# Kernel tuning notes

Hardware: AMD Instinct MI355X
Metric: run time of the kernel (lower is better)

## Reference

```python
import jax, jax.numpy as jnp
import numpy as np

# FlowNetC correlation hyperparameters (from init_kwargs)
PAD = 20
KS = 1
MD = 20
S1 = 1
S2 = 2
MUL = 1


def setup_inputs() -> dict:
    key = jax.random.key(0)
    k1, k2 = jax.random.split(key)
    B, C, H, W = 8, 256, 96, 128
    input1 = jax.random.normal(k1, (B, C, H, W), dtype=jnp.float32)
    input2 = jax.random.normal(k2, (B, C, H, W), dtype=jnp.float32)
    return {"input1": input1, "input2": input2}


def _correlation(in1, in2):
    b, c, h, w = in1.shape
    p1 = jnp.pad(in1, ((0, 0), (0, 0), (PAD, PAD), (PAD, PAD)))
    p2 = jnp.pad(in2, ((0, 0), (0, 0), (PAD, PAD), (PAD, PAD)))
    hp, wp = h + 2 * PAD, w + 2 * PAD
    out_h = (hp - 2 * MD - KS) // S1 + 1
    out_w = (wp - 2 * MD - KS) // S1 + 1
    d = 2 * MD // S2 + 1  # number of displacement steps per axis (21)

    # fixed center region of input1: [b, c, out_h, out_w]
    region1 = p1[:, :, MD:MD + out_h * S1:S1, MD:MD + out_w * S1:S1]

    offs = (jnp.arange(d) - d // 2) * S2  # displacement offsets
    dys, dxs = jnp.meshgrid(offs, offs, indexing='ij')
    dys = dys.reshape(-1)
    dxs = dxs.reshape(-1)

    def step(carry, dydx):
        dy, dx = dydx
        y0 = MD + dy
        x0 = MD + dx
        valid = (y0 >= 0) & (x0 >= 0) & (y0 + out_h * S1 <= hp) & (x0 + out_w * S1 <= wp)
        reg2 = jax.lax.dynamic_slice(
            p2, (0, 0, y0, x0), (b, c, out_h * S1, out_w * S1)
        )[:, :, ::S1, ::S1]
        corr = (region1 * reg2).sum(axis=1) * MUL  # [b, out_h, out_w]
        corr = jnp.where(valid, corr, jnp.zeros_like(corr))
        return carry, corr

    _, chans = jax.lax.scan(step, None, (dys, dxs))  # [d*d, b, out_h, out_w]
    return jnp.transpose(chans, (1, 0, 2, 3))  # [b, d*d, out_h, out_w]


def reference(input1, input2):
    return _correlation(input1, input2)
```

## Files before the change

kernel.cpp:

```cpp
#include <hip/hip_runtime.h>
#include <stdint.h>

#define B_N   8
#define C_N   256
#define H_N   96
#define W_N   128
#define NCK   8
#define ND    21
#define NK    (ND * ND)

typedef __attribute__((ext_vector_type(8))) short short8;
typedef __attribute__((ext_vector_type(4))) float f32x4;

__device__ char zchunk[12288];

__device__ __forceinline__ uint32_t f2bf(float f) {
  uint32_t u = __builtin_bit_cast(uint32_t, f);
  return (u + 0x7fffu + ((u >> 16) & 1u)) >> 16;
}
__device__ __forceinline__ uint32_t packbf(float lo, float hi) {
  return f2bf(lo) | (f2bf(hi) << 16);
}

__global__ __launch_bounds__(256) void prep(const float* __restrict__ in1,
                                            const float* __restrict__ in2,
                                            unsigned short* __restrict__ Apre,
                                            unsigned short* __restrict__ Bpre) {
  __shared__ float tile[32][W_N + 1];
  int blk = blockIdx.x;
  bool isA = blk < 6144;
  int rblk = isA ? blk : blk - 6144;
  int ck = rblk & 7, bi = rblk >> 3;
  int b = bi / H_N, row = bi % H_N;
  const float* src = (isA ? in1 : in2) + ((size_t)(b * C_N + ck * 32) * H_N + row) * W_N;
  int tid = threadIdx.x;
  for (int idx = tid; idx < 32 * W_N; idx += 256) {
    int c = idx >> 7, j = idx & 127;
    tile[c][j] = src[(size_t)c * (H_N * W_N) + j];
  }
  __syncthreads();
  if (isA) {
    uint32_t* dst = (uint32_t*)Apre + (size_t)rblk * 2048;
    for (int q = tid; q < 2048; q += 256) {
      int e2 = q & 3, ln = (q >> 2) & 63, tp = q >> 8;
      int t = tp >> 1, p = tp & 1;
      int m = ln & 15, kg = ln >> 4;
      int c0 = kg * 8 + 2 * e2;
      int j = 32 * t + 2 * m + p;
      dst[q] = packbf(tile[c0][j], tile[c0 + 1][j]);
    }
  } else {
    uint32_t* dst = (uint32_t*)Bpre + (size_t)rblk * 3072;
    for (int q = tid; q < 3072; q += 256) {
      int e2 = q & 3, ln = (q >> 2) & 63, sp = q >> 8;
      int s = sp >> 1, p = sp & 1;
      int m = ln & 15, kg = ln >> 4;
      int c0 = kg * 8 + 2 * e2;
      int x = 32 * s + 2 * m - 20 + p;
      dst[q] = ((unsigned)x < 128u) ? packbf(tile[c0][x], tile[c0 + 1][x]) : 0u;
    }
  }
}

#define DECL_FRAGS(F) short8 F##_a0, F##_a1, F##_bb0, F##_bb1, F##_bb2, F##_bb3, \
                             F##_bb4, F##_bb5, F##_bb6, F##_bb7, F##_bb8, F##_bb9, F##_bb10, F##_bb11

#define LOADF(F, CK) do {                                                        \
  F##_a0 = *(const short8*)(Ap + (size_t)(CK) * 8192);                           \
  F##_a1 = *(const short8*)(Ap + (size_t)(CK) * 8192 + 2048);                    \
  F##_bb0  = *(const short8*)(Bp0 + (size_t)(CK) * bstr0 + 0 * 2048);            \
  F##_bb1  = *(const short8*)(Bp1 + (size_t)(CK) * bstr1 + 0 * 2048);            \
  F##_bb2  = *(const short8*)(Bp2 + (size_t)(CK) * bstr2 + 0 * 2048);            \
  F##_bb3  = *(const short8*)(Bp0 + (size_t)(CK) * bstr0 + 1 * 2048);            \
  F##_bb4  = *(const short8*)(Bp1 + (size_t)(CK) * bstr1 + 1 * 2048);            \
  F##_bb5  = *(const short8*)(Bp2 + (size_t)(CK) * bstr2 + 1 * 2048);            \
  F##_bb6  = *(const short8*)(Bp0 + (size_t)(CK) * bstr0 + 2 * 2048);            \
  F##_bb7  = *(const short8*)(Bp1 + (size_t)(CK) * bstr1 + 2 * 2048);            \
  F##_bb8  = *(const short8*)(Bp2 + (size_t)(CK) * bstr2 + 2 * 2048);            \
  F##_bb9  = *(const short8*)(Bp0 + (size_t)(CK) * bstr0 + 3 * 2048);            \
  F##_bb10 = *(const short8*)(Bp1 + (size_t)(CK) * bstr1 + 3 * 2048);            \
  F##_bb11 = *(const short8*)(Bp2 + (size_t)(CK) * bstr2 + 3 * 2048);            \
} while (0)

#define MF(a, b, c) __builtin_amdgcn_mfma_f32_16x16x32_bf16(a, b, c, 0, 0, 0)
#define COMPUTE(F) do {                                                          \
  acc[0][0][0] = MF(F##_a0, F##_bb0,  acc[0][0][0]);                             \
  acc[0][1][0] = MF(F##_a0, F##_bb1,  acc[0][1][0]);                             \
  acc[0][2][0] = MF(F##_a0, F##_bb2,  acc[0][2][0]);                             \
  acc[0][0][1] = MF(F##_a0, F##_bb3,  acc[0][0][1]);                             \
  acc[1][0][0] = MF(F##_a1, F##_bb3,  acc[1][0][0]);                             \
  acc[0][1][1] = MF(F##_a0, F##_bb4,  acc[0][1][1]);                             \
  acc[1][1][0] = MF(F##_a1, F##_bb4,  acc[1][1][0]);                             \
  acc[0][2][1] = MF(F##_a0, F##_bb5,  acc[0][2][1]);                             \
  acc[1][2][0] = MF(F##_a1, F##_bb5,  acc[1][2][0]);                             \
  acc[0][0][2] = MF(F##_a0, F##_bb6,  acc[0][0][2]);                             \
  acc[1][0][1] = MF(F##_a1, F##_bb6,  acc[1][0][1]);                             \
  acc[0][1][2] = MF(F##_a0, F##_bb7,  acc[0][1][2]);                             \
  acc[1][1][1] = MF(F##_a1, F##_bb7,  acc[1][1][1]);                             \
  acc[0][2][2] = MF(F##_a0, F##_bb8,  acc[0][2][2]);                             \
  acc[1][2][1] = MF(F##_a1, F##_bb8,  acc[1][2][1]);                             \
  acc[1][0][2] = MF(F##_a1, F##_bb9,  acc[1][0][2]);                             \
  acc[1][1][2] = MF(F##_a1, F##_bb10, acc[1][1][2]);                             \
  acc[1][2][2] = MF(F##_a1, F##_bb11, acc[1][2][2]);                             \
} while (0)

__global__ __launch_bounds__(256, 2) void corr_main(const unsigned short* __restrict__ Apre,
                                                    const unsigned short* __restrict__ Bpre,
                                                    float* __restrict__ out) {
  __shared__ float outl[ND][W_N + 1];

  int h = blockIdx.x;
  int l = (h & 7) * 672 + (h >> 3);
  int c = l / 7, q = l - 7 * c;
  int b = c / 96, i0 = c - 96 * b;
  int gidx = 6 - q;
  int i = i0 + 6 * q; if (i >= H_N) i -= H_N;
  int bi = b * H_N + i;
  int dyb = gidx * 3;

  int tid = threadIdx.x;
  int lane = tid & 63, w = tid >> 6;
  int p = w & 1, th = w >> 1;
  int m = lane & 15, kg = lane >> 4;

  f32x4 acc[2][3][3];
#pragma unroll
  for (int a0i = 0; a0i < 2; ++a0i)
#pragma unroll
    for (int a1i = 0; a1i < 3; ++a1i)
#pragma unroll
      for (int a2i = 0; a2i < 3; ++a2i) acc[a0i][a1i][a2i] = {0.f, 0.f, 0.f, 0.f};

  const char* Ap = (const char*)Apre + (size_t)bi * 65536
                   + ((4 * th + p) << 10) + lane * 16;
  const char* Bp0; const char* Bp1; const char* Bp2;
  int bstr0, bstr1, bstr2;
  {
    int y0 = i + 2 * dyb - 20;
#pragma unroll
    for (int g = 0; g < 3; ++g) {
      int y = y0 + 2 * g;
      bool v = (unsigned)y < (unsigned)H_N;
      const char* base = v ? (const char*)Bpre + (size_t)(b * H_N + y) * 98304
                           : (const char*)zchunk;
      const char* bp = base + ((4 * th + p) << 10) + lane * 16;
      int bs = v ? 12288 : 0;
      if (g == 0) { Bp0 = bp; bstr0 = bs; }
      else if (g == 1) { Bp1 = bp; bstr1 = bs; }
      else { Bp2 = bp; bstr2 = bs; }
    }
  }

  DECL_FRAGS(fA);
  DECL_FRAGS(fB);

  LOADF(fA, 0);
  LOADF(fB, 1);
  COMPUTE(fA);
  LOADF(fA, 2);
  COMPUTE(fB);
  LOADF(fB, 3);
  COMPUTE(fA);
  LOADF(fA, 4);
  COMPUTE(fB);
  LOADF(fB, 5);
  COMPUTE(fA);
  LOADF(fA, 6);
  COMPUTE(fB);
  LOADF(fB, 7);
  COMPUTE(fA);
  COMPUTE(fB);

#pragma unroll
  for (int g = 0; g < 3; ++g) {
    __syncthreads();
#pragma unroll
    for (int tt = 0; tt < 2; ++tt) {
      int t = 2 * th + tt;
#pragma unroll
      for (int dl = 0; dl < 3; ++dl) {
#pragma unroll
        for (int r = 0; r < 4; ++r) {
          int a_ = kg * 4 + r;
          int dxi = 16 * dl + m - a_;
          if (dxi >= 0 && dxi <= 20) {
            int j = 2 * (16 * t + a_) + p;
            outl[dxi][j] = acc[tt][g][dl][r];
          }
        }
      }
    }
    __syncthreads();
    int dyi = dyb + g;
    size_t obase = ((size_t)(b * NK + dyi * ND) * H_N + i) * W_N;
    for (int idx = tid; idx < ND * W_N; idx += 256) {
      int dxi = idx >> 7, j = idx & 127;
      out[obase + (size_t)dxi * (H_N * W_N) + j] = outl[dxi][j];
    }
  }
}

__global__ void corr_naive(const float* __restrict__ in1, const float* __restrict__ in2,
                           float* __restrict__ out) {
  size_t o = (size_t)blockIdx.x * 256 + threadIdx.x;
  const size_t total = (size_t)B_N * NK * H_N * W_N;
  if (o >= total) return;
  int j = o & 127;
  int i = (int)((o >> 7) % H_N);
  int k = (int)((o / ((size_t)H_N * W_N)) % NK);
  int b = (int)(o / ((size_t)NK * H_N * W_N));
  int dyi = k / ND, dxi = k % ND;
  int y = i + 2 * dyi - 20, x = j + 2 * dxi - 20;
  float s = 0.f;
  if ((unsigned)y < (unsigned)H_N && (unsigned)x < (unsigned)W_N) {
    const float* p1 = in1 + ((size_t)b * C_N * H_N + i) * W_N + j;
    const float* p2 = in2 + ((size_t)b * C_N * H_N + y) * W_N + x;
    for (int c = 0; c < C_N; ++c)
      s += p1[(size_t)c * H_N * W_N] * p2[(size_t)c * H_N * W_N];
  }
  out[o] = s;
}

extern "C" void kernel_launch(void* const* d_in, const int* in_sizes, int n_in,
                              void* d_out, int out_size, void* d_ws, size_t ws_size,
                              hipStream_t stream) {
  const float* in1 = (const float*)d_in[0];
  const float* in2 = (const float*)d_in[1];
  float* out = (float*)d_out;

  const size_t A_BYTES = (size_t)6144 * 8192;
  const size_t B_BYTES = (size_t)6144 * 12288;
  if (ws_size < A_BYTES + B_BYTES) {
    size_t total = (size_t)B_N * NK * H_N * W_N;
    corr_naive<<<(int)((total + 255) / 256), 256, 0, stream>>>(in1, in2, out);
    return;
  }
  unsigned short* Apre = (unsigned short*)d_ws;
  unsigned short* Bpre = (unsigned short*)((char*)d_ws + A_BYTES);

  prep<<<12288, 256, 0, stream>>>(in1, in2, Apre, Bpre);
  corr_main<<<5376, 256, 0, stream>>>(Apre, Bpre, out);
}
```

Measured before the change: 210.1 us.

## Split correlation into scratch write plus separate permute kernel, add sched barriers

The main correlation kernel now writes its results to a workspace scratch buffer laid out by (b,row,displacement,col), all three displacement groups staged in shared memory at once, then contiguous stores. A second kernel permutes the scratch into the final [b, disp, h, w] layout with float4 copies. Scheduling barriers are added between load/compute stages, and launch bounds drop to one block per SM. The aim is to get contiguous output writes, at the cost of an extra full round trip of the large output through memory, lower occupancy, and more shared memory.

```diff
diff --git a/kernel.cpp b/kernel.cpp
--- a/kernel.cpp
+++ b/kernel.cpp
@@ -104,73 +104,112 @@
   acc[1][2][2] = MF(F##_a1, F##_bb11, acc[1][2][2]);                             \
 } while (0)
 
-__global__ __launch_bounds__(256, 2) void corr_main(const unsigned short* __restrict__ Apre,
-                                                    const unsigned short* __restrict__ Bpre,
-                                                    float* __restrict__ out) {
+#define SB() __builtin_amdgcn_sched_barrier(0)
+
+#define MAIN_PROLOGUE                                                            \
+  int h = blockIdx.x;                                                            \
+  int l = (h & 7) * 672 + (h >> 3);                                              \
+  int c = l / 7, q = l - 7 * c;                                                  \
+  int b = c / 96, i0 = c - 96 * b;                                               \
+  int gidx = 6 - q;                                                              \
+  int i = i0 + 6 * q; if (i >= H_N) i -= H_N;                                    \
+  int bi = b * H_N + i;                                                          \
+  int dyb = gidx * 3;                                                            \
+  int tid = threadIdx.x;                                                         \
+  int lane = tid & 63, w = tid >> 6;                                             \
+  int p = w & 1, th = w >> 1;                                                    \
+  int m = lane & 15, kg = lane >> 4;                                             \
+  f32x4 acc[2][3][3];                                                            \
+  _Pragma("unroll")                                                              \
+  for (int a0i = 0; a0i < 2; ++a0i)                                              \
+    _Pragma("unroll")                                                            \
+    for (int a1i = 0; a1i < 3; ++a1i)                                            \
+      _Pragma("unroll")                                                          \
+      for (int a2i = 0; a2i < 3; ++a2i) acc[a0i][a1i][a2i] = {0.f, 0.f, 0.f, 0.f}; \
+  const char* Ap = (const char*)Apre + (size_t)bi * 65536                        \
+                   + ((4 * th + p) << 10) + lane * 16;                           \
+  const char* Bp0; const char* Bp1; const char* Bp2;                             \
+  int bstr0, bstr1, bstr2;                                                       \
+  {                                                                              \
+    int y0 = i + 2 * dyb - 20;                                                   \
+    _Pragma("unroll")                                                            \
+    for (int g = 0; g < 3; ++g) {                                                \
+      int y = y0 + 2 * g;                                                        \
+      bool v = (unsigned)y < (unsigned)H_N;                                      \
+      const char* base = v ? (const char*)Bpre + (size_t)(b * H_N + y) * 98304   \
+                           : (const char*)zchunk;                                \
+      const char* bp = base + ((4 * th + p) << 10) + lane * 16;                  \
+      int bs = v ? 12288 : 0;                                                    \
+      if (g == 0) { Bp0 = bp; bstr0 = bs; }                                      \
+      else if (g == 1) { Bp1 = bp; bstr1 = bs; }                                 \
+      else { Bp2 = bp; bstr2 = bs; }                                             \
+    }                                                                            \
+  }                                                                              \
+  DECL_FRAGS(fA);                                                                \
+  DECL_FRAGS(fB);                                                                \
+  LOADF(fA, 0); LOADF(fB, 1); SB();                                              \
+  COMPUTE(fA); LOADF(fA, 2); SB();                                               \
+  COMPUTE(fB); LOADF(fB, 3); SB();                                               \
+  COMPUTE(fA); LOADF(fA, 4); SB();                                               \
+  COMPUTE(fB); LOADF(fB, 5); SB();                                               \
+  COMPUTE(fA); LOADF(fA, 6); SB();                                               \
+  COMPUTE(fB); LOADF(fB, 7); SB();                                               \
+  COMPUTE(fA); SB();                                                             \
+  COMPUTE(fB);
+
+__global__ __launch_bounds__(256, 1) void corr_split(const unsigned short* __restrict__ Apre,
+                                                     const unsigned short* __restrict__ Bpre,
+                                                     float* __restrict__ scr) {
+  __shared__ float outl3[3][ND][W_N + 1];
+  MAIN_PROLOGUE
+#pragma unroll
+  for (int g = 0; g < 3; ++g) {
+#pragma unroll
+    for (int tt = 0; tt < 2; ++tt) {
+      int t = 2 * th + tt;
+#pragma unroll
+      for (int dl = 0; dl < 3; ++dl) {
+#pragma unroll
+        for (int r = 0; r < 4; ++r) {
+          int a_ = kg * 4 + r;
+          int dxi = 16 * dl + m - a_;
+          if (dxi >= 0 && dxi <= 20) {
+            int j = 2 * (16 * t + a_) + p;
+            outl3[g][dxi][j] = acc[tt][g][dl][r];
+          }
+        }
+      }
+    }
+  }
+  __syncthreads();
+  size_t sbase = ((size_t)bi * NK + (size_t)dyb * ND) * W_N;
+  for (int idx = tid; idx < 3 * ND * W_N; idx += 256) {
+    int g = idx / (ND * W_N), r2 = idx - g * (ND * W_N);
+    int dxi = r2 >> 7, j = r2 & 127;
+    scr[sbase + (size_t)((g * ND + dxi) << 7) + j] = outl3[g][dxi][j];
+  }
+}
+
+__global__ __launch_bounds__(256) void permute_out(const float* __restrict__ scr,
+                                                   float* __restrict__ out) {
+  int blk = blockIdx.x;
+  int b = blk & 7, k = blk >> 3;
+  int tid = threadIdx.x;
+  int ii = tid >> 5, jj = tid & 31;
+#pragma unroll 4
+  for (int i8 = 0; i8 < 12; ++i8) {
+    int i = i8 * 8 + ii;
+    const float4* s = (const float4*)(scr + ((size_t)(b * H_N + i) * NK + k) * W_N) + jj;
+    float4 v = *s;
+    *((float4*)(out + ((size_t)(b * NK + k) * H_N + i) * W_N) + jj) = v;
+  }
+}
+
+__global__ __launch_bounds__(256, 1) void corr_fused(const unsigned short* __restrict__ Apre,
+                                                     const unsigned short* __restrict__ Bpre,
+                                                     float* __restrict__ out) {
   __shared__ float outl[ND][W_N + 1];
-
-  int h = blockIdx.x;
-  int l = (h & 7) * 672 + (h >> 3);
-  int c = l / 7, q = l - 7 * c;
-  int b = c / 96, i0 = c - 96 * b;
-  int gidx = 6 - q;
-  int i = i0 + 6 * q; if (i >= H_N) i -= H_N;
-  int bi = b * H_N + i;
-  int dyb = gidx * 3;
-
-  int tid = threadIdx.x;
-  int lane = tid & 63, w = tid >> 6;
-  int p = w & 1, th = w >> 1;
-  int m = lane & 15, kg = lane >> 4;
-
-  f32x4 acc[2][3][3];
-#pragma unroll
-  for (int a0i = 0; a0i < 2; ++a0i)
-#pragma unroll
-    for (int a1i = 0; a1i < 3; ++a1i)
-#pragma unroll
-      for (int a2i = 0; a2i < 3; ++a2i) acc[a0i][a1i][a2i] = {0.f, 0.f, 0.f, 0.f};
-
-  const char* Ap = (const char*)Apre + (size_t)bi * 65536
-                   + ((4 * th + p) << 10) + lane * 16;
-  const char* Bp0; const char* Bp1; const char* Bp2;
-  int bstr0, bstr1, bstr2;
-  {
-    int y0 = i + 2 * dyb - 20;
-#pragma unroll
-    for (int g = 0; g < 3; ++g) {
-      int y = y0 + 2 * g;
-      bool v = (unsigned)y < (unsigned)H_N;
-      const char* base = v ? (const char*)Bpre + (size_t)(b * H_N + y) * 98304
-                           : (const char*)zchunk;
-      const char* bp = base + ((4 * th + p) << 10) + lane * 16;
-      int bs = v ? 12288 : 0;
-      if (g == 0) { Bp0 = bp; bstr0 = bs; }
-      else if (g == 1) { Bp1 = bp; bstr1 = bs; }
-      else { Bp2 = bp; bstr2 = bs; }
-    }
-  }
-
-  DECL_FRAGS(fA);
-  DECL_FRAGS(fB);
-
-  LOADF(fA, 0);
-  LOADF(fB, 1);
-  COMPUTE(fA);
-  LOADF(fA, 2);
-  COMPUTE(fB);
-  LOADF(fB, 3);
-  COMPUTE(fA);
-  LOADF(fA, 4);
-  COMPUTE(fB);
-  LOADF(fB, 5);
-  COMPUTE(fA);
-  LOADF(fA, 6);
-  COMPUTE(fB);
-  LOADF(fB, 7);
-  COMPUTE(fA);
-  COMPUTE(fB);
-
+  MAIN_PROLOGUE
 #pragma unroll
   for (int g = 0; g < 3; ++g) {
     __syncthreads();
@@ -230,6 +269,7 @@
 
   const size_t A_BYTES = (size_t)6144 * 8192;
   const size_t B_BYTES = (size_t)6144 * 12288;
+  const size_t SCR_BYTES = (size_t)768 * NK * W_N * 4;
   if (ws_size < A_BYTES + B_BYTES) {
     size_t total = (size_t)B_N * NK * H_N * W_N;
     corr_naive<<<(int)((total + 255) / 256), 256, 0, stream>>>(in1, in2, out);
@@ -239,5 +279,12 @@
   unsigned short* Bpre = (unsigned short*)((char*)d_ws + A_BYTES);
 
   prep<<<12288, 256, 0, stream>>>(in1, in2, Apre, Bpre);
-  corr_main<<<5376, 256, 0, stream>>>(Apre, Bpre, out);
-}
+
+  if (ws_size >= A_BYTES + B_BYTES + SCR_BYTES) {
+    float* scr = (float*)((char*)d_ws + A_BYTES + B_BYTES);
+    corr_split<<<5376, 256, 0, stream>>>(Apre, Bpre, scr);
+    permute_out<<<3528, 256, 0, stream>>>(scr, out);
+  } else {
+    corr_fused<<<5376, 256, 0, stream>>>(Apre, Bpre, out);
+  }
+}
```

Result: slower. 274.5 us (+30.7%).
